# Performance work log

Hardware: AMD Instinct MI355X
Metric: run time of the kernel (lower is better)

## Reference

```python
import jax, jax.numpy as jnp
import numpy as np

N_NODES = 10000
N_EDGES = 320000
D_FEAT = 128          # per-node feature dim -> in_dim = 2*D_FEAT = 256
OUT_DIM = 128
SCALES = 3


def setup_inputs() -> dict:
    key = jax.random.key(0)
    ks = jax.random.split(key, 7)
    node_features = jax.random.normal(ks[0], (N_NODES, D_FEAT), dtype=jnp.float32)
    temporal_info = jax.random.normal(ks[1], (N_NODES,), dtype=jnp.float32)
    in_dim_p1 = 2 * D_FEAT + 1  # 257: concat(src, dest) + temporal gap
    W1 = jax.random.normal(ks[2], (SCALES, in_dim_p1, OUT_DIM), dtype=jnp.float32) * 0.05
    b1 = jax.random.normal(ks[3], (SCALES, OUT_DIM), dtype=jnp.float32) * 0.05
    W2 = jax.random.normal(ks[4], (SCALES, OUT_DIM, OUT_DIM), dtype=jnp.float32) * 0.05
    b2 = jax.random.normal(ks[5], (SCALES, OUT_DIM), dtype=jnp.float32) * 0.05
    edge_index = jax.random.randint(ks[6], (2, N_EDGES), 0, N_NODES, dtype=jnp.int64)
    return {
        "node_features": node_features,
        "temporal_info": temporal_info,
        "W1": W1, "b1": b1, "W2": W2, "b2": b2,
        "edge_index": edge_index,
    }


def reference(node_features, temporal_info, W1, b1, W2, b2, edge_index):
    src, dest = edge_index[0], edge_index[1]
    # gather node pairs + temporal gap -> [E, 2*D+1]
    gap = (temporal_info[src] - temporal_info[dest])[:, None]
    edge_features = jnp.concatenate(
        [node_features[src], node_features[dest], gap], axis=-1)
    # all scales' 2-layer MLPs in one batched einsum; s = scale axis
    h = jax.nn.relu(jnp.einsum('ef,sfo->seo', edge_features, W1) + b1[:, None, :])
    tokens = jnp.einsum('seo,sop->sep', h, W2) + b2[:, None, :]  # [S, E, OUT]
    return tokens.mean(axis=0)  # mean over scales -> [E, OUT]
```

## Files before the change

### kernel.cpp

```cpp
#include <hip/hip_runtime.h>
#include <stdint.h>

#define NN 10000
#define NE 320000
#define DF 128
#define OD 128
#define NS 3

typedef __attribute__((ext_vector_type(8))) short bf16x8;
typedef __attribute__((ext_vector_type(16))) float f32x16;

static __device__ __forceinline__ uint32_t f2bf(float f) {
  uint32_t u = __float_as_uint(f);
  return (u + 0x7FFFu + ((u >> 16) & 1u)) >> 16;
}
static __device__ __forceinline__ float bflo(uint32_t u) { return __uint_as_float(u << 16); }
static __device__ __forceinline__ float bfhi(uint32_t u) { return __uint_as_float(u & 0xFFFF0000u); }

static __device__ __forceinline__ uint32_t relu2(uint32_t a, uint32_t d) {
  float f0 = fmaxf(bflo(a) + bflo(d), 0.0f);
  float f1 = fmaxf(bfhi(a) + bfhi(d), 0.0f);
  return f2bf(f0) | (f2bf(f1) << 16);
}

static __device__ __forceinline__ void lds_barrier() {
  asm volatile("s_waitcnt lgkmcnt(0)" ::: "memory");
  __builtin_amdgcn_s_barrier();
}

__global__ __launch_bounds__(256) void prep_w2(
    const float* __restrict__ W2, const float* __restrict__ b2,
    unsigned short* __restrict__ w2t, float* __restrict__ bmean)
{
  int tid = blockIdx.x * 256 + threadIdx.x;
  if (tid < NS * OD * OD) {
    int s = tid / (OD * OD);
    int r = tid % (OD * OD);
    int k = r / OD;
    int n = r % OD;
    w2t[(s * OD + n) * OD + k] = (unsigned short)f2bf(W2[tid]);
  }
  if (tid < OD) bmean[tid] = (b2[tid] + b2[OD + tid] + b2[2 * OD + tid]) * (1.0f / 3.0f);
}

__global__ __launch_bounds__(256) void node_proj(
    const float* __restrict__ nf, const float* __restrict__ temporal,
    const float* __restrict__ W1, const float* __restrict__ b1,
    unsigned short* __restrict__ Qsrc, unsigned short* __restrict__ Qdst)
{
  __shared__ unsigned short Asm[8 * 64 * 8];
  __shared__ unsigned short Bsm[4 * 8 * 64 * 8];
  __shared__ float tsh[32];

  const int t = threadIdx.x;
  const int c = blockIdx.y;
  const int s = c >> 1, proj = c & 1;

  {
    int o = t & 127, qh = t >> 7;
    const float* wbase = W1 + (size_t)(s * 257 + proj * 128) * OD + o;
    int nt = o >> 5, lnlo = o & 31;
    #pragma unroll
    for (int r = 0; r < 8; r++) {
      int kh = qh * 8 + r;
      float v[8];
      #pragma unroll
      for (int j = 0; j < 8; j++) v[j] = wbase[(size_t)(kh * 8 + j) * OD];
      uint32_t pk[4];
      #pragma unroll
      for (int i = 0; i < 4; i++) pk[i] = f2bf(v[2 * i]) | (f2bf(v[2 * i + 1]) << 16);
      int q = kh >> 1, half = kh & 1;
      uint32_t* d = (uint32_t*)(Bsm + ((nt * 8 + q) * 64 + half * 32 + lnlo) * 8);
      d[0] = pk[0]; d[1] = pk[1]; d[2] = pk[2]; d[3] = pk[3];
    }
  }

  const int lane = t & 63, w = t >> 6;
  const int o = w * 32 + (lane & 31);
  const float w1gv = W1[(size_t)(s * 257 + 256) * OD + o];
  const float b1v = b1[s * OD + o];
  unsigned short* Qt = (proj == 0) ? Qsrc : Qdst;
  const int m = t >> 3, j16 = t & 7;

  for (int it = 0; it < 8; it++) {
    const int m0 = (blockIdx.x * 8 + it) * 32;
    if (m0 >= NN) break;

    if (t < 32) tsh[t] = (m0 + t < NN) ? temporal[m0 + t] : 0.0f;

    {
      int node = m0 + m;
      float v[16];
      if (node < NN) {
        const float4* p = (const float4*)(nf + (size_t)node * DF + j16 * 16);
        #pragma unroll
        for (int i = 0; i < 4; i++) {
          float4 x = p[i];
          v[4 * i] = x.x; v[4 * i + 1] = x.y; v[4 * i + 2] = x.z; v[4 * i + 3] = x.w;
        }
      } else {
        #pragma unroll
        for (int i = 0; i < 16; i++) v[i] = 0.0f;
      }
      uint32_t pk[8];
      #pragma unroll
      for (int i = 0; i < 8; i++) pk[i] = f2bf(v[2 * i]) | (f2bf(v[2 * i + 1]) << 16);
      uint32_t* d0 = (uint32_t*)(Asm + (j16 * 64 + (m ^ j16)) * 8);
      uint32_t* d1 = (uint32_t*)(Asm + (j16 * 64 + ((32 + m) ^ j16)) * 8);
      d0[0] = pk[0]; d0[1] = pk[1]; d0[2] = pk[2]; d0[3] = pk[3];
      d1[0] = pk[4]; d1[1] = pk[5]; d1[2] = pk[6]; d1[3] = pk[7];
    }
    __syncthreads();

    f32x16 C;
    #pragma unroll
    for (int i = 0; i < 16; i++) C[i] = 0.0f;
    #pragma unroll
    for (int q = 0; q < 8; q++) {
      bf16x8 a = *(const bf16x8*)(Asm + (q * 64 + (lane ^ q)) * 8);
      bf16x8 b = *(const bf16x8*)(Bsm + ((w * 8 + q) * 64 + lane) * 8);
      C = __builtin_amdgcn_mfma_f32_32x32x16_bf16(a, b, C, 0, 0, 0);
    }

    #pragma unroll
    for (int r = 0; r < 16; r++) {
      int row = (r & 3) + 8 * (r >> 2) + 4 * (lane >> 5);
      int node = m0 + row;
      if (node < NN) {
        float val = C[r];
        if (proj == 0) val += b1v + tsh[row] * w1gv;
        else           val -= tsh[row] * w1gv;
        Qt[(size_t)node * (NS * OD) + s * OD + o] = (unsigned short)f2bf(val);
      }
    }
    __syncthreads();
  }
}

#define EGRID 500
#define ENT   20

static __device__ __forceinline__ void gather12(
    uint4* G, const unsigned short* __restrict__ Qsrc,
    const unsigned short* __restrict__ Qdst, int sn, int dn, int j16)
{
  const unsigned short* ps = Qsrc + (size_t)sn * (NS * OD) + j16 * 16;
  const unsigned short* pd = Qdst + (size_t)dn * (NS * OD) + j16 * 16;
  #pragma unroll
  for (int s = 0; s < NS; s++) {
    G[4 * s + 0] = *(const uint4*)(ps + s * OD);
    G[4 * s + 1] = *(const uint4*)(ps + s * OD + 8);
    G[4 * s + 2] = *(const uint4*)(pd + s * OD);
    G[4 * s + 3] = *(const uint4*)(pd + s * OD + 8);
  }
}

static __device__ __forceinline__ void produce_h(
    unsigned short* HS, const uint4* G, int m, int j16)
{
  #pragma unroll
  for (int s = 0; s < NS; s++) {
    uint4 a0 = G[4 * s + 0], a1 = G[4 * s + 1];
    uint4 d0 = G[4 * s + 2], d1 = G[4 * s + 3];
    uint4 w0, w1;
    w0.x = relu2(a0.x, d0.x); w0.y = relu2(a0.y, d0.y);
    w0.z = relu2(a0.z, d0.z); w0.w = relu2(a0.w, d0.w);
    w1.x = relu2(a1.x, d1.x); w1.y = relu2(a1.y, d1.y);
    w1.z = relu2(a1.z, d1.z); w1.w = relu2(a1.w, d1.w);
    *(uint4*)(HS + ((s * 8 + j16) * 64 + (m ^ j16)) * 8) = w0;
    *(uint4*)(HS + ((s * 8 + j16) * 64 + ((32 + m) ^ j16)) * 8) = w1;
  }
}

__global__ __launch_bounds__(256) void edge_mlp(
    const unsigned short* __restrict__ Qsrc, const unsigned short* __restrict__ Qdst,
    const unsigned short* __restrict__ W2T, const float* __restrict__ bmean,
    const int* __restrict__ ei, float* __restrict__ out)
{
  __shared__ unsigned short hsm[2][NS * 8 * 64 * 8];

  const int t = threadIdx.x;
  const int lane = t & 63, w = t >> 6;
  const int nlo = lane & 31, khi = lane >> 5;

  bf16x8 bfrag[NS][8];
  {
    int n = w * 32 + nlo;
    #pragma unroll
    for (int s = 0; s < NS; s++) {
      const unsigned short* base = W2T + ((s * OD + n) * OD + khi * 8);
      #pragma unroll
      for (int q = 0; q < 8; q++)
        bfrag[s][q] = *(const bf16x8*)(base + q * 16);
    }
  }
  const float bmv = bmean[w * 32 + nlo];
  const int m = t >> 3, j16 = t & 7;

  auto EB = [&](int k) -> int {
    int kk = (k < ENT) ? k : (ENT - 1);
    return (blockIdx.x + (kk >> 2) * EGRID) * 128 + (kk & 3) * 32;
  };

  int sn, dn;
  uint4 GA[12], GB[12];

  { int e = EB(0) + m; sn = ei[e]; dn = ei[NE + e]; }
  gather12(GB, Qsrc, Qdst, sn, dn, j16);
  { int e = EB(1) + m; sn = ei[e]; dn = ei[NE + e]; }
  gather12(GA, Qsrc, Qdst, sn, dn, j16);
  { int e = EB(2) + m; sn = ei[e]; dn = ei[NE + e]; }
  produce_h(hsm[0], GB, m, j16);
  lds_barrier();

#define STEP(K, GC, GN, P) do {                                               \
    if ((K) + 2 < ENT) gather12(GN, Qsrc, Qdst, sn, dn, j16);                 \
    { int e3 = EB((K) + 3) + m; sn = ei[e3]; dn = ei[NE + e3]; }              \
    f32x16 C;                                                                 \
    _Pragma("unroll") for (int i = 0; i < 16; i++) C[i] = 0.0f;               \
    __builtin_amdgcn_s_setprio(1);                                            \
    _Pragma("unroll") for (int s = 0; s < NS; s++) {                          \
      _Pragma("unroll") for (int q = 0; q < 8; q++) {                         \
        bf16x8 a = *(const bf16x8*)(hsm[P] + ((s * 8 + q) * 64 + (lane ^ q)) * 8); \
        C = __builtin_amdgcn_mfma_f32_32x32x16_bf16(a, bfrag[s][q], C, 0, 0, 0);   \
      }                                                                       \
    }                                                                         \
    __builtin_amdgcn_s_setprio(0);                                            \
    if ((K) + 1 < ENT) produce_h(hsm[(P) ^ 1], GC, m, j16);                   \
    const int e0 = EB(K);                                                     \
    _Pragma("unroll") for (int r = 0; r < 16; r++) {                          \
      int row = (r & 3) + 8 * (r >> 2) + 4 * khi;                             \
      __builtin_nontemporal_store(C[r] * (1.0f / 3.0f) + bmv,                 \
          &out[(size_t)(e0 + row) * OD + w * 32 + nlo]);                      \
    }                                                                         \
    lds_barrier();                                                            \
  } while (0)

  #pragma unroll 1
  for (int kk = 0; kk < ENT; kk += 2) {
    STEP(kk,     GA, GB, 0);
    STEP(kk + 1, GB, GA, 1);
  }
#undef STEP
}

extern "C" void kernel_launch(void* const* d_in, const int* in_sizes, int n_in,
                              void* d_out, int out_size, void* d_ws, size_t ws_size,
                              hipStream_t stream) {
  const float* nf       = (const float*)d_in[0];
  const float* temporal = (const float*)d_in[1];
  const float* W1       = (const float*)d_in[2];
  const float* b1       = (const float*)d_in[3];
  const float* W2       = (const float*)d_in[4];
  const float* b2       = (const float*)d_in[5];
  const int*   ei       = (const int*)d_in[6];
  float* out = (float*)d_out;

  char* ws = (char*)d_ws;
  unsigned short* Qsrc = (unsigned short*)ws;
  unsigned short* Qdst = (unsigned short*)(ws + 7680000);
  unsigned short* W2T  = (unsigned short*)(ws + 15360000);
  float*          bmv  = (float*)(ws + 15360000 + 98304);

  prep_w2 <<<dim3(192),     dim3(256), 0, stream>>>(W2, b2, W2T, bmv);
  node_proj<<<dim3(40, 6),  dim3(256), 0, stream>>>(nf, temporal, W1, b1, Qsrc, Qdst);
  edge_mlp <<<dim3(EGRID),  dim3(256), 0, stream>>>(Qsrc, Qdst, W2T, bmv, ei, out);
}
```

Before: 294.4 us.

## Fold W2 prep into node_proj, shorten edge blocks, use packed bf16 convert

Removes the separate prep_w2 launch by having node_proj blocks also transpose and convert W2 and compute the mean bias. The edge kernel goes from a persistent 500-block grid with 20 tiles each and a double-buffered LDS pipeline to 2500 blocks of 4 tiles with a single LDS buffer, prefetching the next gather while the current tile computes. The ReLU pack uses the hardware v_cvt_pk_bf16_f32 instruction instead of manual rounding. The trade-off is that each block must reload W2 fragments more often, its pipeline is shorter and less overlapped, and LDS use per block is lower, which may allow more occupancy.

```diff
diff --git a/kernel.cpp b/kernel.cpp
--- a/kernel.cpp
+++ b/kernel.cpp
@@ -20,7 +20,9 @@
 static __device__ __forceinline__ uint32_t relu2(uint32_t a, uint32_t d) {
   float f0 = fmaxf(bflo(a) + bflo(d), 0.0f);
   float f1 = fmaxf(bfhi(a) + bfhi(d), 0.0f);
-  return f2bf(f0) | (f2bf(f1) << 16);
+  uint32_t r;
+  asm("v_cvt_pk_bf16_f32 %0, %1, %2" : "=v"(r) : "v"(f0), "v"(f1));
+  return r;
 }
 
 static __device__ __forceinline__ void lds_barrier() {
@@ -28,24 +30,11 @@
   __builtin_amdgcn_s_barrier();
 }
 
-__global__ __launch_bounds__(256) void prep_w2(
-    const float* __restrict__ W2, const float* __restrict__ b2,
-    unsigned short* __restrict__ w2t, float* __restrict__ bmean)
-{
-  int tid = blockIdx.x * 256 + threadIdx.x;
-  if (tid < NS * OD * OD) {
-    int s = tid / (OD * OD);
-    int r = tid % (OD * OD);
-    int k = r / OD;
-    int n = r % OD;
-    w2t[(s * OD + n) * OD + k] = (unsigned short)f2bf(W2[tid]);
-  }
-  if (tid < OD) bmean[tid] = (b2[tid] + b2[OD + tid] + b2[2 * OD + tid]) * (1.0f / 3.0f);
-}
-
 __global__ __launch_bounds__(256) void node_proj(
     const float* __restrict__ nf, const float* __restrict__ temporal,
     const float* __restrict__ W1, const float* __restrict__ b1,
+    const float* __restrict__ W2, const float* __restrict__ b2,
+    unsigned short* __restrict__ w2t, float* __restrict__ bmean,
     unsigned short* __restrict__ Qsrc, unsigned short* __restrict__ Qdst)
 {
   __shared__ unsigned short Asm[8 * 64 * 8];
@@ -55,6 +44,18 @@
   const int t = threadIdx.x;
   const int c = blockIdx.y;
   const int s = c >> 1, proj = c & 1;
+
+  {
+    int o = (blockIdx.y * 40 + blockIdx.x) * 256 + t;
+    if (o < NS * OD * OD) {
+      int ss = o / (OD * OD);
+      int r = o % (OD * OD);
+      int k = r / OD;
+      int n = r % OD;
+      w2t[(ss * OD + n) * OD + k] = (unsigned short)f2bf(W2[o]);
+    }
+    if (o < OD) bmean[o] = (b2[o] + b2[OD + o] + b2[2 * OD + o]) * (1.0f / 3.0f);
+  }
 
   {
     int o = t & 127, qh = t >> 7;
@@ -137,47 +138,12 @@
   }
 }
 
-#define EGRID 500
-#define ENT   20
-
-static __device__ __forceinline__ void gather12(
-    uint4* G, const unsigned short* __restrict__ Qsrc,
-    const unsigned short* __restrict__ Qdst, int sn, int dn, int j16)
-{
-  const unsigned short* ps = Qsrc + (size_t)sn * (NS * OD) + j16 * 16;
-  const unsigned short* pd = Qdst + (size_t)dn * (NS * OD) + j16 * 16;
-  #pragma unroll
-  for (int s = 0; s < NS; s++) {
-    G[4 * s + 0] = *(const uint4*)(ps + s * OD);
-    G[4 * s + 1] = *(const uint4*)(ps + s * OD + 8);
-    G[4 * s + 2] = *(const uint4*)(pd + s * OD);
-    G[4 * s + 3] = *(const uint4*)(pd + s * OD + 8);
-  }
-}
-
-static __device__ __forceinline__ void produce_h(
-    unsigned short* HS, const uint4* G, int m, int j16)
-{
-  #pragma unroll
-  for (int s = 0; s < NS; s++) {
-    uint4 a0 = G[4 * s + 0], a1 = G[4 * s + 1];
-    uint4 d0 = G[4 * s + 2], d1 = G[4 * s + 3];
-    uint4 w0, w1;
-    w0.x = relu2(a0.x, d0.x); w0.y = relu2(a0.y, d0.y);
-    w0.z = relu2(a0.z, d0.z); w0.w = relu2(a0.w, d0.w);
-    w1.x = relu2(a1.x, d1.x); w1.y = relu2(a1.y, d1.y);
-    w1.z = relu2(a1.z, d1.z); w1.w = relu2(a1.w, d1.w);
-    *(uint4*)(HS + ((s * 8 + j16) * 64 + (m ^ j16)) * 8) = w0;
-    *(uint4*)(HS + ((s * 8 + j16) * 64 + ((32 + m) ^ j16)) * 8) = w1;
-  }
-}
-
 __global__ __launch_bounds__(256) void edge_mlp(
     const unsigned short* __restrict__ Qsrc, const unsigned short* __restrict__ Qdst,
     const unsigned short* __restrict__ W2T, const float* __restrict__ bmean,
     const int* __restrict__ ei, float* __restrict__ out)
 {
-  __shared__ unsigned short hsm[2][NS * 8 * 64 * 8];
+  __shared__ unsigned short hsm[NS * 8 * 64 * 8];
 
   const int t = threadIdx.x;
   const int lane = t & 63, w = t >> 6;
@@ -195,39 +161,54 @@
     }
   }
   const float bmv = bmean[w * 32 + nlo];
+
   const int m = t >> 3, j16 = t & 7;
 
-  auto EB = [&](int k) -> int {
-    int kk = (k < ENT) ? k : (ENT - 1);
-    return (blockIdx.x + (kk >> 2) * EGRID) * 128 + (kk & 3) * 32;
-  };
-
-  int sn, dn;
+  int sn[4], dn[4];
+  #pragma unroll
+  for (int tt = 0; tt < 4; tt++) {
+    int e = blockIdx.x * 128 + tt * 32 + m;
+    sn[tt] = ei[e];
+    dn[tt] = ei[NE + e];
+  }
+
   uint4 GA[12], GB[12];
 
-  { int e = EB(0) + m; sn = ei[e]; dn = ei[NE + e]; }
-  gather12(GB, Qsrc, Qdst, sn, dn, j16);
-  { int e = EB(1) + m; sn = ei[e]; dn = ei[NE + e]; }
-  gather12(GA, Qsrc, Qdst, sn, dn, j16);
-  { int e = EB(2) + m; sn = ei[e]; dn = ei[NE + e]; }
-  produce_h(hsm[0], GB, m, j16);
-  lds_barrier();
-
-#define STEP(K, GC, GN, P) do {                                               \
-    if ((K) + 2 < ENT) gather12(GN, Qsrc, Qdst, sn, dn, j16);                 \
-    { int e3 = EB((K) + 3) + m; sn = ei[e3]; dn = ei[NE + e3]; }              \
+#define GATHER(DST, TT) do {                                                  \
+    const unsigned short* ps = Qsrc + (size_t)sn[TT] * (NS * OD) + j16 * 16;  \
+    const unsigned short* pd = Qdst + (size_t)dn[TT] * (NS * OD) + j16 * 16;  \
+    _Pragma("unroll") for (int s = 0; s < NS; s++) {                          \
+      DST[4 * s + 0] = *(const uint4*)(ps + s * OD);                          \
+      DST[4 * s + 1] = *(const uint4*)(ps + s * OD + 8);                      \
+      DST[4 * s + 2] = *(const uint4*)(pd + s * OD);                          \
+      DST[4 * s + 3] = *(const uint4*)(pd + s * OD + 8);                      \
+    } } while (0)
+
+#define STEP(TT, GC, GN) do {                                                 \
+    const int e0 = blockIdx.x * 128 + (TT) * 32;                              \
+    _Pragma("unroll") for (int s = 0; s < NS; s++) {                          \
+      uint4 a0 = GC[4 * s + 0], a1 = GC[4 * s + 1];                           \
+      uint4 d0 = GC[4 * s + 2], d1 = GC[4 * s + 3];                           \
+      uint4 w0, w1;                                                           \
+      w0.x = relu2(a0.x, d0.x); w0.y = relu2(a0.y, d0.y);                     \
+      w0.z = relu2(a0.z, d0.z); w0.w = relu2(a0.w, d0.w);                     \
+      w1.x = relu2(a1.x, d1.x); w1.y = relu2(a1.y, d1.y);                     \
+      w1.z = relu2(a1.z, d1.z); w1.w = relu2(a1.w, d1.w);                     \
+      *(uint4*)(hsm + ((s * 8 + j16) * 64 + (m ^ j16)) * 8) = w0;             \
+      *(uint4*)(hsm + ((s * 8 + j16) * 64 + ((32 + m) ^ j16)) * 8) = w1;      \
+    }                                                                         \
+    if ((TT) < 3) GATHER(GN, (TT) + 1);                                       \
+    lds_barrier();                                                            \
     f32x16 C;                                                                 \
     _Pragma("unroll") for (int i = 0; i < 16; i++) C[i] = 0.0f;               \
     __builtin_amdgcn_s_setprio(1);                                            \
     _Pragma("unroll") for (int s = 0; s < NS; s++) {                          \
       _Pragma("unroll") for (int q = 0; q < 8; q++) {                         \
-        bf16x8 a = *(const bf16x8*)(hsm[P] + ((s * 8 + q) * 64 + (lane ^ q)) * 8); \
-        C = __builtin_amdgcn_mfma_f32_32x32x16_bf16(a, bfrag[s][q], C, 0, 0, 0);   \
+        bf16x8 a = *(const bf16x8*)(hsm + ((s * 8 + q) * 64 + (lane ^ q)) * 8); \
+        C = __builtin_amdgcn_mfma_f32_32x32x16_bf16(a, bfrag[s][q], C, 0, 0, 0); \
       }                                                                       \
     }                                                                         \
     __builtin_amdgcn_s_setprio(0);                                            \
-    if ((K) + 1 < ENT) produce_h(hsm[(P) ^ 1], GC, m, j16);                   \
-    const int e0 = EB(K);                                                     \
     _Pragma("unroll") for (int r = 0; r < 16; r++) {                          \
       int row = (r & 3) + 8 * (r >> 2) + 4 * khi;                             \
       __builtin_nontemporal_store(C[r] * (1.0f / 3.0f) + bmv,                 \
@@ -236,12 +217,14 @@
     lds_barrier();                                                            \
   } while (0)
 
-  #pragma unroll 1
-  for (int kk = 0; kk < ENT; kk += 2) {
-    STEP(kk,     GA, GB, 0);
-    STEP(kk + 1, GB, GA, 1);
-  }
+  GATHER(GA, 0);
+  STEP(0, GA, GB);
+  STEP(1, GB, GA);
+  STEP(2, GA, GB);
+  STEP(3, GB, GA);
+
 #undef STEP
+#undef GATHER
 }
 
 extern "C" void kernel_launch(void* const* d_in, const int* in_sizes, int n_in,
@@ -262,7 +245,7 @@
   unsigned short* W2T  = (unsigned short*)(ws + 15360000);
   float*          bmv  = (float*)(ws + 15360000 + 98304);
 
-  prep_w2 <<<dim3(192),     dim3(256), 0, stream>>>(W2, b2, W2T, bmv);
-  node_proj<<<dim3(40, 6),  dim3(256), 0, stream>>>(nf, temporal, W1, b1, Qsrc, Qdst);
-  edge_mlp <<<dim3(EGRID),  dim3(256), 0, stream>>>(Qsrc, Qdst, W2T, bmv, ei, out);
-}
+  node_proj<<<dim3(40, 6), dim3(256), 0, stream>>>(
+      nf, temporal, W1, b1, W2, b2, W2T, bmv, Qsrc, Qdst);
+  edge_mlp <<<dim3(2500),  dim3(256), 0, stream>>>(Qsrc, Qdst, W2T, bmv, ei, out);
+}
```

After: 261.9 us. 1.12x faster.
